# Optimization experiments

Measured on AMD Instinct MI355X. Metric: run time of the kernel, lower is better.

## Reference

```python
import jax, jax.numpy as jnp
import numpy as np

N = 30000      # nodes
E = 480000     # edges
G = 256        # g_dim
H = 8          # heads
D = G // H     # head dim
SCALE = G ** (-0.5)
LN_EPS = 1e-5


def setup_inputs() -> dict:
    key = jax.random.key(0)
    k0, k1, k2, k3 = jax.random.split(key, 4)
    s = jax.random.normal(k0, (N, G), dtype=jnp.float32)
    src = jax.random.randint(k1, (E,), 0, N, dtype=jnp.int32)
    dst = jax.random.randint(k2, (E,), 0, N, dtype=jnp.int32)
    # learned params: fused qkv projection (no bias) + LayerNorm affine
    Wqkv = jax.random.normal(k3, (G, 3 * G), dtype=jnp.float32) * (G ** -0.5)
    gamma = jnp.ones((G,), dtype=jnp.float32)
    beta = jnp.zeros((G,), dtype=jnp.float32)
    return {"s": s, "Wqkv": Wqkv, "gamma": gamma, "beta": beta, "src": src, "dst": dst}


def _segment_softmax(logits, seg, num_segments):
    # numerically stable softmax over edges grouped by destination node,
    # elementwise over trailing (h, d) dims — matches dgl.edge_softmax
    m = jax.ops.segment_max(logits, seg, num_segments=num_segments)
    e = jnp.exp(logits - m[seg])
    z = jax.ops.segment_sum(e, seg, num_segments=num_segments)
    return e / z[seg]


def reference(s, Wqkv, gamma, beta, src, dst):
    # LayerNorm over feature dim
    mu = jnp.mean(s, axis=-1, keepdims=True)
    var = jnp.mean((s - mu) ** 2, axis=-1, keepdims=True)
    x = (s - mu) * jax.lax.rsqrt(var + LN_EPS) * gamma + beta
    # fused qkv projection, split into heads
    qkv = x @ Wqkv                                  # [N, 3G]
    q, k, v = jnp.split(qkv, 3, axis=-1)
    q = q.reshape(N, H, D)
    k = k.reshape(N, H, D)
    v = v.reshape(N, H, D)
    # per-edge elementwise attention: u_mul_v('q','k') * scale -> [E, H, D]
    att = q[src] * k[dst] * SCALE
    att = _segment_softmax(att, dst, N)
    # weighted scatter-sum aggregation: sum_e v[src_e] * att_e into dst_e
    msg = v[src] * att                              # [E, H, D]
    rst = jax.ops.segment_sum(msg, dst, num_segments=N)  # [N, H, D]
    return rst.reshape(N, G)
```

## Files before the change

### kernel.cpp

```cpp
#include <hip/hip_runtime.h>
#include <hip/hip_fp16.h>
#include <string.h>

#define NN 30000
#define NE 480000
#define CAP 96
#define KSC (0.0625f * 1.44269504f)

typedef __attribute__((ext_vector_type(8))) _Float16 f16x8;
typedef __attribute__((ext_vector_type(4))) float f32x4;
typedef __attribute__((ext_vector_type(4))) int i32x4;
typedef __attribute__((ext_vector_type(2))) unsigned int u32x2;

__device__ __forceinline__ unsigned short f2h(float f) {
    _Float16 h = (_Float16)f;
    unsigned short u;
    memcpy(&u, &h, 2);
    return u;
}

__device__ __forceinline__ void gload16(const void* g, void* l) {
    __builtin_amdgcn_global_load_lds(
        (const __attribute__((address_space(1))) unsigned int*)g,
        (__attribute__((address_space(3))) unsigned int*)l, 16, 0, 0);
}

#define LNB 7500
#define WTB 48
__global__ __launch_bounds__(256) void prologue_kernel(const float* __restrict__ s,
                                                       const float* __restrict__ gamma,
                                                       const float* __restrict__ beta,
                                                       unsigned short* __restrict__ xh,
                                                       const float* __restrict__ W,
                                                       unsigned short* __restrict__ WT,
                                                       const int* __restrict__ src,
                                                       const int* __restrict__ dst,
                                                       int* __restrict__ cursor,
                                                       unsigned short* __restrict__ col,
                                                       unsigned int* __restrict__ qvu) {
    const int bid = blockIdx.x;
    const int tid = threadIdx.x;
    if (bid < LNB) {
        const int wave = tid >> 6, lane = tid & 63;
        const int n = bid * 4 + wave;
        const f32x4 v = *(const f32x4*)(s + (size_t)n * 256 + lane * 4);
        float sum = v[0] + v[1] + v[2] + v[3];
        float sq  = v[0]*v[0] + v[1]*v[1] + v[2]*v[2] + v[3]*v[3];
        #pragma unroll
        for (int o = 1; o < 64; o <<= 1) {
            sum += __shfl_xor(sum, o, 64);
            sq  += __shfl_xor(sq,  o, 64);
        }
        const float mu  = sum * (1.0f / 256.0f);
        const float var = sq  * (1.0f / 256.0f) - mu * mu;
        const float rs  = rsqrtf(var + 1e-5f);
        const f32x4 g4 = *(const f32x4*)(gamma + lane * 4);
        const f32x4 b4 = *(const f32x4*)(beta  + lane * 4);
        union { unsigned short us[4]; u32x2 u; } o_;
        #pragma unroll
        for (int j = 0; j < 4; j++)
            o_.us[j] = f2h((v[j] - mu) * rs * g4[j] + b4[j]);
        *(u32x2*)(xh + (size_t)n * 256 + lane * 4) = o_.u;
    } else if (bid < LNB + WTB) {
        const int t  = bid - LNB;
        const int k0 = (t & 3) * 64;
        const int n0 = (t >> 2) * 64;
        __shared__ float tsm[64][65];
        const int tx = tid & 63, ty = tid >> 6;
        #pragma unroll
        for (int r = 0; r < 16; r++) {
            const int kr = ty + r * 4;
            tsm[kr][tx] = W[(size_t)(k0 + kr) * 768 + n0 + tx];
        }
        __syncthreads();
        #pragma unroll
        for (int r = 0; r < 16; r++) {
            const int nr = ty + r * 4;
            WT[(size_t)(n0 + nr) * 256 + k0 + tx] = f2h(tsm[tx][nr]);
        }
    } else if (bid == LNB + WTB) {
        const int x = tid >> 5, j = tid & 31;
        qvu[((size_t)x * (NN + 1) + NN) * 32 + j] = 0u;
    } else {
        const int e = (bid - (LNB + WTB + 1)) * 256 + tid;
        if (e < NE) {
            const int d = dst[e];
            const int slot = atomicAdd(&cursor[d], 1);
            if (slot < CAP) col[d * CAP + slot] = (unsigned short)src[e];
        }
    }
}

#define BM 128
#define BN 128
#define BK 64
#define CSTRIDE 136
#define MTILES 235

__global__ __launch_bounds__(256) void gemm_kernel(const unsigned short* __restrict__ A,
                                                   const unsigned short* __restrict__ B,
                                                   unsigned short* __restrict__ qv,
                                                   unsigned short* __restrict__ kb) {
    const int f   = blockIdx.x;
    const int xcd = f & 7;
    const int i   = f >> 3;
    const int bmi = xcd * 30 + i / 6;
    if (bmi >= MTILES) return;
    const int bm = bmi * BM;
    const int by = i % 6;
    const int bn = by * BN;

    __shared__ unsigned short smem[BM * CSTRIDE];
    unsigned short* As = smem;
    unsigned short* Bs = smem + 8192;

    const int tid  = threadIdx.x;
    const int lane = tid & 63;
    const int wave = tid >> 6;
    const int wm = (wave & 1) * 64;
    const int wn = (wave >> 1) * 64;
    const int l16  = lane & 15;
    const int quad = lane >> 4;

    const int srow0 = wave * 8 + (lane >> 3);
    const int ko    = (lane & 7) * 8;

    f32x4 acc[4][4] = {};

    for (int kt = 0; kt < 256; kt += BK) {
        #pragma unroll
        for (int j = 0; j < 4; j++) {
            const int r = srow0 + 32 * j;
            int gmA = bm + r; if (gmA >= NN) gmA = NN - 1;
            gload16(A + (size_t)gmA * 256 + kt + ko, &As[(wave * 8 + 32 * j) * 64]);
            gload16(B + (size_t)(bn + r) * 256 + kt + ko, &Bs[(wave * 8 + 32 * j) * 64]);
        }
        __syncthreads();

        #pragma unroll
        for (int ks = 0; ks < 2; ks++) {
            f16x8 af[4], bfr[4];
            #pragma unroll
            for (int ii = 0; ii < 4; ii++)
                af[ii]  = *(const f16x8*)(&As[(wm + ii * 16 + l16) * 64 + ks * 32 + quad * 8]);
            #pragma unroll
            for (int jj = 0; jj < 4; jj++)
                bfr[jj] = *(const f16x8*)(&Bs[(wn + jj * 16 + l16) * 64 + ks * 32 + quad * 8]);
            #pragma unroll
            for (int ii = 0; ii < 4; ii++)
                #pragma unroll
                for (int jj = 0; jj < 4; jj++)
                    acc[ii][jj] = __builtin_amdgcn_mfma_f32_16x16x32_f16(af[ii], bfr[jj], acc[ii][jj], 0, 0, 0);
        }
        __syncthreads();
    }

    #pragma unroll
    for (int ii = 0; ii < 4; ii++)
        #pragma unroll
        for (int jj = 0; jj < 4; jj++)
            #pragma unroll
            for (int r = 0; r < 4; r++)
                smem[(wm + ii * 16 + quad * 4 + r) * CSTRIDE + wn + jj * 16 + l16] =
                    f2h(acc[ii][jj][r]);
    __syncthreads();

    const int sector  = by >> 1;
    const int colhalf = (by & 1) * 128;
    const int row  = tid >> 1;
    const int cseg = (tid & 1) * 64;
    const int grow = bm + row;
    if (grow < NN) {
        #pragma unroll
        for (int k = 0; k < 8; k++) {
            i32x4 val = *(const i32x4*)(&smem[row * CSTRIDE + cseg + k * 8]);
            const int c = colhalf + cseg + k * 8;
            const int x = c >> 5;
            if (sector == 1) {
                *(i32x4*)(kb + ((size_t)x * NN + grow) * 32 + (c & 31)) = val;
            } else {
                unsigned short* base = qv + ((size_t)x * (NN + 1) + grow) * 64
                                       + ((c & 31) >> 2) * 8 + (sector == 2 ? 4 : 0);
                u32x2 lo, hi;
                lo.x = (unsigned int)val[0]; lo.y = (unsigned int)val[1];
                hi.x = (unsigned int)val[2]; hi.y = (unsigned int)val[3];
                *(u32x2*)(base)     = lo;
                *(u32x2*)(base + 8) = hi;
            }
        }
    }
}

#define SSTRIDE 100

union U { unsigned int u; __half2 h; };

__global__ __launch_bounds__(256) void edge_kernel(const unsigned short* __restrict__ qv,
                                                   const unsigned short* __restrict__ ks,
                                                   const int* __restrict__ cursor,
                                                   const unsigned short* __restrict__ col,
                                                   float* __restrict__ out) {
    const int x   = blockIdx.x;
    const int nb  = blockIdx.y * 32;
    const int tid = threadIdx.x;
    const int w   = tid >> 6;
    const int lane = tid & 63;

    __shared__ int scol[32 * SSTRIDE];
    __shared__ int sdegR[32], sdegS[32], snode[32];

    if (tid < 32) {
        const int n0 = nb + tid;
        int d = (n0 < NN) ? cursor[n0] : 0;
        sdegR[tid] = (d > CAP) ? CAP : d;
    }
    __syncthreads();
    if (tid < 32) {
        const int d = sdegR[tid];
        int r = 0;
        #pragma unroll
        for (int j = 0; j < 32; ++j) {
            const int dj = sdegR[j];
            r += (dj < d) || (dj == d && j < tid);
        }
        sdegS[r] = d;
        snode[r] = nb + tid;
    }
    __syncthreads();
    {
        const unsigned int* colu = (const unsigned int*)col;
        #pragma unroll
        for (int j = 0; j < 6; j++) {
            const int t2 = tid + j * 256;
            const int nd = t2 / 48;
            const int ps = t2 - nd * 48;
            const int sn = snode[nd];
            const int deg = sdegS[nd];
            const int row = (sn < NN) ? sn : 0;
            const unsigned int u = colu[row * 48 + ps];
            int e0 = (int)(u & 0xffffu);
            int e1 = (int)(u >> 16);
            e0 = (2 * ps     < deg) ? e0 : NN;
            e1 = (2 * ps + 1 < deg) ? e1 : NN;
            scol[nd * SSTRIDE + 2 * ps]     = e0 << 7;
            scol[nd * SSTRIDE + 2 * ps + 1] = e1 << 7;
        }
    }
    __syncthreads();

    const int g  = lane >> 3;
    const int cq = lane & 7;
    const int li = w * 8 + g;
    const int m  = snode[li];
    const int msafe = (m < NN) ? m : 0;

    const int mydeg = sdegS[li];
    const int dmax4 = (sdegS[w * 8 + 7] + 3) & ~3;

    u32x2 kraw = *(const u32x2*)(ks + ((size_t)x * NN + msafe) * 32 + 4 * cq);
    U t0, t1; t0.u = kraw.x; t1.u = kraw.y;
    const __half2 ksc2 = __float2half2_rn(KSC);
    const __half2 kkA = __hmul2(t0.h, ksc2);
    const __half2 kkB = __hmul2(t1.h, ksc2);

    const char* qvp = (const char*)qv + (size_t)x * (NN + 1) * 128 + cq * 16;
    const int* myscol = &scol[li * SSTRIDE];

    __half2 zA = __float2half2_rn(0.0f), zB = __float2half2_rn(0.0f);
    __half2 aA = __float2half2_rn(0.0f), aB = __float2half2_rn(0.0f);

#define EDGE_COMPUTE(d4) do {                                        \
        U q01, q23, v01, v23;                                        \
        q01.u = (unsigned int)(d4)[0];                               \
        q23.u = (unsigned int)(d4)[1];                               \
        v01.u = (unsigned int)(d4)[2];                               \
        v23.u = (unsigned int)(d4)[3];                               \
        const __half2 w0 = h2exp2(__hmul2(q01.h, kkA));              \
        const __half2 w1 = h2exp2(__hmul2(q23.h, kkB));              \
        zA = __hadd2(zA, w0);                                        \
        aA = __hfma2(w0, v01.h, aA);                                 \
        zB = __hadd2(zB, w1);                                        \
        aB = __hfma2(w1, v23.h, aB);                                 \
    } while (0)

    if (dmax4 > 0) {
        i32x4 off4 = *(const i32x4*)(&myscol[0]);
        i32x4 dc0 = *(const i32x4*)(qvp + off4[0]);
        i32x4 dc1 = *(const i32x4*)(qvp + off4[1]);
        i32x4 dc2 = *(const i32x4*)(qvp + off4[2]);
        i32x4 dc3 = *(const i32x4*)(qvp + off4[3]);
        for (int i = 4; i < dmax4; i += 4) {
            const i32x4 offn = *(const i32x4*)(&myscol[i]);
            const i32x4 dn0 = *(const i32x4*)(qvp + offn[0]);
            const i32x4 dn1 = *(const i32x4*)(qvp + offn[1]);
            const i32x4 dn2 = *(const i32x4*)(qvp + offn[2]);
            const i32x4 dn3 = *(const i32x4*)(qvp + offn[3]);
            EDGE_COMPUTE(dc0); EDGE_COMPUTE(dc1);
            EDGE_COMPUTE(dc2); EDGE_COMPUTE(dc3);
            dc0 = dn0; dc1 = dn1; dc2 = dn2; dc3 = dn3;
        }
        EDGE_COMPUTE(dc0); EDGE_COMPUTE(dc1);
        EDGE_COMPUTE(dc2); EDGE_COMPUTE(dc3);
    }
#undef EDGE_COMPUTE

    const float npad = (float)(dmax4 - mydeg);
    f32x4 o;
    const float z0 = __low2float(zA)  - npad;
    const float z1 = __high2float(zA) - npad;
    const float z2 = __low2float(zB)  - npad;
    const float z3 = __high2float(zB) - npad;
    o[0] = (mydeg > 0) ? __low2float(aA)  / z0 : 0.0f;
    o[1] = (mydeg > 0) ? __high2float(aA) / z1 : 0.0f;
    o[2] = (mydeg > 0) ? __low2float(aB)  / z2 : 0.0f;
    o[3] = (mydeg > 0) ? __high2float(aB) / z3 : 0.0f;
    if (m < NN)
        *(f32x4*)(out + (size_t)m * 256 + x * 32 + 4 * cq) = o;
}

extern "C" void kernel_launch(void* const* d_in, const int* in_sizes, int n_in,
                              void* d_out, int out_size, void* d_ws, size_t ws_size,
                              hipStream_t stream) {
    const float* s     = (const float*)d_in[0];
    const float* Wqkv  = (const float*)d_in[1];
    const float* gamma = (const float*)d_in[2];
    const float* beta  = (const float*)d_in[3];
    const int*   src   = (const int*)d_in[4];
    const int*   dst   = (const int*)d_in[5];
    float* out = (float*)d_out;

    char* ws = (char*)d_ws;
    unsigned short* xh   = (unsigned short*)(ws);
    unsigned short* WT   = (unsigned short*)(ws + 15360000);
    unsigned short* qv   = (unsigned short*)(ws + 15753216);
    unsigned short* ks   = (unsigned short*)(ws + 46474240);
    int*            cur  = (int*)(ws + 61834240);
    unsigned short* col  = (unsigned short*)(ws + 61954240);

    hipMemsetAsync(cur, 0, NN * sizeof(int), stream);

    const int scatter_blocks = (NE + 255) / 256;
    prologue_kernel<<<LNB + WTB + 1 + scatter_blocks, 256, 0, stream>>>(
        s, gamma, beta, xh, Wqkv, WT, src, dst, cur, col, (unsigned int*)qv);
    gemm_kernel<<<1440, 256, 0, stream>>>(xh, WT, qv, ks);
    edge_kernel<<<dim3(8, (NN + 31) / 32), 256, 0, stream>>>(qv, ks, cur, col, out);
}
```

Before: 200.6 us.

## Move edge scatter into GEMM launch, pad cursors, simplify edge gather loop

The edge-bucketing scatter (atomic slot claims and col writes) moves from the prologue kernel into extra blocks appended to the GEMM launch, so it runs alongside the matmul instead of the LayerNorm phase. Per-node cursors are spaced 32 ints apart, which is meant to reduce atomic contention and false sharing on cache lines, at the cost of a larger memset and a sparser cursor read in the edge kernel. The edge kernel's hand-written software-pipelined gather loop becomes a plain unrolled loop, leaving load scheduling to the compiler and giving up the explicit prefetch.

```diff
diff --git a/kernel.cpp b/kernel.cpp
--- a/kernel.cpp
+++ b/kernel.cpp
@@ -5,6 +5,7 @@
 #define NN 30000
 #define NE 480000
 #define CAP 96
+#define CURP 32
 #define KSC (0.0625f * 1.44269504f)
 
 typedef __attribute__((ext_vector_type(8))) _Float16 f16x8;
@@ -33,10 +34,6 @@
                                                        unsigned short* __restrict__ xh,
                                                        const float* __restrict__ W,
                                                        unsigned short* __restrict__ WT,
-                                                       const int* __restrict__ src,
-                                                       const int* __restrict__ dst,
-                                                       int* __restrict__ cursor,
-                                                       unsigned short* __restrict__ col,
                                                        unsigned int* __restrict__ qvu) {
     const int bid = blockIdx.x;
     const int tid = threadIdx.x;
@@ -78,16 +75,9 @@
             const int nr = ty + r * 4;
             WT[(size_t)(n0 + nr) * 256 + k0 + tx] = f2h(tsm[tx][nr]);
         }
-    } else if (bid == LNB + WTB) {
+    } else {
         const int x = tid >> 5, j = tid & 31;
         qvu[((size_t)x * (NN + 1) + NN) * 32 + j] = 0u;
-    } else {
-        const int e = (bid - (LNB + WTB + 1)) * 256 + tid;
-        if (e < NE) {
-            const int d = dst[e];
-            const int slot = atomicAdd(&cursor[d], 1);
-            if (slot < CAP) col[d * CAP + slot] = (unsigned short)src[e];
-        }
     }
 }
 
@@ -96,12 +86,26 @@
 #define BK 64
 #define CSTRIDE 136
 #define MTILES 235
+#define GEMMB 1440
 
 __global__ __launch_bounds__(256) void gemm_kernel(const unsigned short* __restrict__ A,
                                                    const unsigned short* __restrict__ B,
                                                    unsigned short* __restrict__ qv,
-                                                   unsigned short* __restrict__ kb) {
-    const int f   = blockIdx.x;
+                                                   unsigned short* __restrict__ kb,
+                                                   const int* __restrict__ src,
+                                                   const int* __restrict__ dst,
+                                                   int* __restrict__ cursor,
+                                                   unsigned short* __restrict__ col) {
+    const int f = blockIdx.x;
+    if (f >= GEMMB) {
+        const int e = (f - GEMMB) * 256 + threadIdx.x;
+        if (e < NE) {
+            const int d = dst[e];
+            const int slot = atomicAdd(&cursor[d * CURP], 1);
+            if (slot < CAP) col[d * CAP + slot] = (unsigned short)src[e];
+        }
+        return;
+    }
     const int xcd = f & 7;
     const int i   = f >> 3;
     const int bmi = xcd * 30 + i / 6;
@@ -211,7 +215,7 @@
 
     if (tid < 32) {
         const int n0 = nb + tid;
-        int d = (n0 < NN) ? cursor[n0] : 0;
+        int d = (n0 < NN) ? cursor[n0 * CURP] : 0;
         sdegR[tid] = (d > CAP) ? CAP : d;
     }
     __syncthreads();
@@ -269,40 +273,24 @@
     __half2 zA = __float2half2_rn(0.0f), zB = __float2half2_rn(0.0f);
     __half2 aA = __float2half2_rn(0.0f), aB = __float2half2_rn(0.0f);
 
-#define EDGE_COMPUTE(d4) do {                                        \
-        U q01, q23, v01, v23;                                        \
-        q01.u = (unsigned int)(d4)[0];                               \
-        q23.u = (unsigned int)(d4)[1];                               \
-        v01.u = (unsigned int)(d4)[2];                               \
-        v23.u = (unsigned int)(d4)[3];                               \
-        const __half2 w0 = h2exp2(__hmul2(q01.h, kkA));              \
-        const __half2 w1 = h2exp2(__hmul2(q23.h, kkB));              \
-        zA = __hadd2(zA, w0);                                        \
-        aA = __hfma2(w0, v01.h, aA);                                 \
-        zB = __hadd2(zB, w1);                                        \
-        aB = __hfma2(w1, v23.h, aB);                                 \
-    } while (0)
-
-    if (dmax4 > 0) {
-        i32x4 off4 = *(const i32x4*)(&myscol[0]);
-        i32x4 dc0 = *(const i32x4*)(qvp + off4[0]);
-        i32x4 dc1 = *(const i32x4*)(qvp + off4[1]);
-        i32x4 dc2 = *(const i32x4*)(qvp + off4[2]);
-        i32x4 dc3 = *(const i32x4*)(qvp + off4[3]);
-        for (int i = 4; i < dmax4; i += 4) {
-            const i32x4 offn = *(const i32x4*)(&myscol[i]);
-            const i32x4 dn0 = *(const i32x4*)(qvp + offn[0]);
-            const i32x4 dn1 = *(const i32x4*)(qvp + offn[1]);
-            const i32x4 dn2 = *(const i32x4*)(qvp + offn[2]);
-            const i32x4 dn3 = *(const i32x4*)(qvp + offn[3]);
-            EDGE_COMPUTE(dc0); EDGE_COMPUTE(dc1);
-            EDGE_COMPUTE(dc2); EDGE_COMPUTE(dc3);
-            dc0 = dn0; dc1 = dn1; dc2 = dn2; dc3 = dn3;
-        }
-        EDGE_COMPUTE(dc0); EDGE_COMPUTE(dc1);
-        EDGE_COMPUTE(dc2); EDGE_COMPUTE(dc3);
-    }
-#undef EDGE_COMPUTE
+    for (int i = 0; i < dmax4; i += 4) {
+        const i32x4 off4 = *(const i32x4*)(&myscol[i]);
+        #pragma unroll
+        for (int j = 0; j < 4; j++) {
+            const i32x4 d4 = *(const i32x4*)(qvp + off4[j]);
+            U q01, q23, v01, v23;
+            q01.u = (unsigned int)d4[0];
+            q23.u = (unsigned int)d4[1];
+            v01.u = (unsigned int)d4[2];
+            v23.u = (unsigned int)d4[3];
+            const __half2 w0 = h2exp2(__hmul2(q01.h, kkA));
+            const __half2 w1 = h2exp2(__hmul2(q23.h, kkB));
+            zA = __hadd2(zA, w0);
+            aA = __hfma2(w0, v01.h, aA);
+            zB = __hadd2(zB, w1);
+            aB = __hfma2(w1, v23.h, aB);
+        }
+    }
 
     const float npad = (float)(dmax4 - mydeg);
     f32x4 o;
@@ -335,13 +323,14 @@
     unsigned short* qv   = (unsigned short*)(ws + 15753216);
     unsigned short* ks   = (unsigned short*)(ws + 46474240);
     int*            cur  = (int*)(ws + 61834240);
-    unsigned short* col  = (unsigned short*)(ws + 61954240);
-
-    hipMemsetAsync(cur, 0, NN * sizeof(int), stream);
-
+    unsigned short* col  = (unsigned short*)(ws + 65674240);
+
+    hipMemsetAsync(cur, 0, (size_t)NN * CURP * sizeof(int), stream);
+
+    prologue_kernel<<<LNB + WTB + 1, 256, 0, stream>>>(
+        s, gamma, beta, xh, Wqkv, WT, (unsigned int*)qv);
     const int scatter_blocks = (NE + 255) / 256;
-    prologue_kernel<<<LNB + WTB + 1 + scatter_blocks, 256, 0, stream>>>(
-        s, gamma, beta, xh, Wqkv, WT, src, dst, cur, col, (unsigned int*)qv);
-    gemm_kernel<<<1440, 256, 0, stream>>>(xh, WT, qv, ks);
+    gemm_kernel<<<GEMMB + scatter_blocks, 256, 0, stream>>>(
+        xh, WT, qv, ks, src, dst, cur, col);
     edge_kernel<<<dim3(8, (NN + 31) / 32), 256, 0, stream>>>(qv, ks, cur, col, out);
 }
```

Result: faster. 190.5 us (-5.0%).
